# Optimization experiments

Hardware: AMD Instinct MI355X
Metric: run time of the kernel (lower is better)

## Reference

```python
import jax, jax.numpy as jnp
import numpy as np

N_NODES, D_NODE = 100000, 128
N_EDGES, D_EDGE = 1000000, 32
D_IN = 2 * D_NODE + D_EDGE  # 288
H1, H2, D_OUT = 128, 64, 1


def setup_inputs() -> dict:
    key = jax.random.key(0)
    ks = jax.random.split(key, 9)
    x = jax.random.normal(ks[0], (N_NODES, D_NODE), dtype=jnp.float32)
    edge_index = jax.random.randint(ks[1], (2, N_EDGES), 0, N_NODES, dtype=jnp.int64)
    edge_features = jax.random.normal(ks[2], (N_EDGES, D_EDGE), dtype=jnp.float32)
    def lin(kw, kb, fan_in, fan_out):
        bound = 1.0 / np.sqrt(fan_in)
        W = jax.random.uniform(kw, (fan_in, fan_out), minval=-bound, maxval=bound, dtype=jnp.float32)
        b = jax.random.uniform(kb, (fan_out,), minval=-bound, maxval=bound, dtype=jnp.float32)
        return W, b
    W1, b1 = lin(ks[3], ks[4], D_IN, H1)
    W2, b2 = lin(ks[5], ks[6], H1, H2)
    W3, b3 = lin(ks[7], ks[8], H2, D_OUT)
    return {"x": x, "edge_index": edge_index, "edge_features": edge_features,
            "W1": W1, "b1": b1, "W2": W2, "b2": b2, "W3": W3, "b3": b3}


def reference(x, edge_index, edge_features, W1, b1, W2, b2, W3, b3):
    origin, destination = edge_index[0], edge_index[1]
    # [E, 2*D_NODE + D_EDGE]
    z = jnp.concatenate([x[origin], x[destination], edge_features], axis=1)
    z = jax.nn.leaky_relu(z @ W1 + b1)  # negative_slope=0.01, matches torch default
    z = jax.nn.leaky_relu(z @ W2 + b2)
    z = z @ W3 + b3
    return z.reshape(-1)
```

## Files before the change

kernel.cpp:

```cpp
#include <hip/hip_runtime.h>

#define N_NODES 100000
#define N_EDGES 1000000

typedef __attribute__((ext_vector_type(8))) short bf16x8;
typedef __attribute__((ext_vector_type(4))) float f32x4;
typedef __attribute__((ext_vector_type(4))) unsigned u32x4;

static __device__ __forceinline__ short f2bf(float f) {
    unsigned u = __float_as_uint(f);
    u = (u + 0x7fffu + ((u >> 16) & 1u)) >> 16;
    return (short)u;
}
static __device__ __forceinline__ float bf2f(unsigned short s) {
    return __uint_as_float(((unsigned)s) << 16);
}
static __device__ __forceinline__ float lrelu(float x) {
    return fmaxf(x, 0.01f * x);
}
static __device__ __forceinline__ unsigned cvtpk(float lo, float hi) {
    unsigned r;
    asm("v_cvt_pk_bf16_f32 %0, %1, %2" : "=v"(r) : "v"(lo), "v"(hi));
    return r;
}

__global__ __launch_bounds__(256) void precompute_mfma(
    const float* __restrict__ x, const float* __restrict__ W1,
    const float* __restrict__ b1, unsigned short* __restrict__ Pb,
    unsigned short* __restrict__ Qb)
{
    const int t    = threadIdx.x;
    const int lane = t & 63;
    const int w    = t >> 6;
    const int q    = lane >> 4;
    const int n15  = lane & 15;
    const int chb  = 64 * w;

    bf16x8 afrag[4][4];
    #pragma unroll
    for (int mtl = 0; mtl < 4; ++mtl) {
        const int ch = chb + 16 * mtl + n15;
        const float* wcol = (ch < 128) ? (W1 + ch) : (W1 + 128 * 128 + (ch - 128));
        #pragma unroll
        for (int ks = 0; ks < 4; ++ks)
            #pragma unroll
            for (int j = 0; j < 8; ++j)
                afrag[mtl][ks][j] = f2bf(wcol[(size_t)(32 * ks + 8 * q + j) * 128]);
    }
    float b1r[16];
    #pragma unroll
    for (int mtl = 0; mtl < 4; ++mtl)
        #pragma unroll
        for (int r = 0; r < 4; ++r) {
            const int ch = chb + 16 * mtl + 4 * q + r;
            b1r[mtl * 4 + r] = (ch < 128) ? b1[ch] : 0.0f;
        }

    unsigned short* tbase = (w < 2) ? Pb : Qb;
    const int mtb = 4 * (w & 1);

    for (int tile = blockIdx.x; tile < N_NODES / 16; tile += gridDim.x) {
        const int n0 = tile * 16;
        const float* xrow = x + (size_t)(n0 + n15) * 128;

        bf16x8 bfr[4];
        #pragma unroll
        for (int ks = 0; ks < 4; ++ks) {
            f32x4 xa = *(const f32x4*)(xrow + 32 * ks + 8 * q);
            f32x4 xb = *(const f32x4*)(xrow + 32 * ks + 8 * q + 4);
            u32x4 bu;
            bu[0] = cvtpk(xa[0], xa[1]);
            bu[1] = cvtpk(xa[2], xa[3]);
            bu[2] = cvtpk(xb[0], xb[1]);
            bu[3] = cvtpk(xb[2], xb[3]);
            bfr[ks] = __builtin_bit_cast(bf16x8, bu);
        }
        #pragma unroll
        for (int mtl = 0; mtl < 4; ++mtl) {
            f32x4 acc = {0.f, 0.f, 0.f, 0.f};
            #pragma unroll
            for (int ks = 0; ks < 4; ++ks)
                acc = __builtin_amdgcn_mfma_f32_16x16x32_bf16(afrag[mtl][ks], bfr[ks], acc, 0, 0, 0);
            unsigned* dst = (unsigned*)(tbase + (size_t)(n0 + n15) * 128 + q * 32 + (mtb + mtl) * 4);
            dst[0] = cvtpk(acc[0] + b1r[mtl * 4 + 0], acc[1] + b1r[mtl * 4 + 1]);
            dst[1] = cvtpk(acc[2] + b1r[mtl * 4 + 2], acc[3] + b1r[mtl * 4 + 3]);
        }
    }
}

__global__ __launch_bounds__(256, 3) void edge_mfma(
    const int* __restrict__ ei, const float* __restrict__ ef,
    const float* __restrict__ W1, const float* __restrict__ W2,
    const float* __restrict__ b2, const float* __restrict__ W3,
    const float* __restrict__ b3, const unsigned short* __restrict__ Pb,
    const unsigned short* __restrict__ Qb, float* __restrict__ out)
{
    __shared__ unsigned short w2s[16 * 64 * 8];
    __shared__ unsigned short a1s[8 * 64 * 8];
    const int t    = threadIdx.x;
    const int lane = t & 63;
    const int w    = t >> 6;
    const int q    = lane >> 4;
    const int n15  = lane & 15;

    #pragma unroll
    for (int i = 0; i < 2; ++i) {
        const int mt = 2 * w + i;
        bf16x8 f;
        #pragma unroll
        for (int j = 0; j < 8; ++j)
            f[j] = f2bf(W1[(size_t)(256 + 8 * q + j) * 128 + 16 * mt + n15]);
        *(bf16x8*)&a1s[(mt * 64 + lane) * 8] = f;
    }

    {
        const int mt2 = w;
        #pragma unroll
        for (int ks = 0; ks < 4; ++ks) {
            bf16x8 f;
            #pragma unroll
            for (int j = 0; j < 8; ++j) {
                const int ch = 32 * ks + ((j < 4) ? (4 * q + j) : (16 + 4 * q + (j - 4)));
                f[j] = f2bf(W2[(size_t)ch * 64 + 16 * mt2 + n15]);
            }
            *(bf16x8*)&w2s[(((mt2 << 2) | ks) * 64 + lane) * 8] = f;
        }
    }

    unsigned b2w3[16];
    #pragma unroll
    for (int mt2 = 0; mt2 < 4; ++mt2)
        #pragma unroll
        for (int r = 0; r < 4; ++r) {
            const int ch = 16 * mt2 + 4 * q + r;
            b2w3[mt2 * 4 + r] = (unsigned)(unsigned short)f2bf(b2[ch])
                              | ((unsigned)(unsigned short)f2bf(W3[ch]) << 16);
        }
    const float b3v = b3[0];

    __syncthreads();

    const int nTiles  = N_EDGES / 16;
    const int wid     = blockIdx.x * 4 + w;
    const int wstride = gridDim.x * 4;
    if (wid >= nTiles) return;

    int t0 = wid, t1 = t0 + wstride, t2 = t1 + wstride;
    bool h1 = t1 < nTiles, h2 = t2 < nTiles;

    int oi0, di0, oi1, di1, oi2, di2;
    f32x4 ea0, eb0, ea1, eb1, ea2, eb2;
    {
        const int e0 = t0 * 16;
        oi0 = ei[e0 + n15];
        di0 = ei[N_EDGES + e0 + n15];
        ea0 = *(const f32x4*)(ef + (size_t)(e0 + n15) * 32 + 8 * q);
        eb0 = *(const f32x4*)(ef + (size_t)(e0 + n15) * 32 + 8 * q + 4);
    }
    oi1 = oi0; di1 = di0; ea1 = ea0; eb1 = eb0;
    if (h1) {
        const int e1 = t1 * 16;
        oi1 = ei[e1 + n15];
        di1 = ei[N_EDGES + e1 + n15];
        ea1 = *(const f32x4*)(ef + (size_t)(e1 + n15) * 32 + 8 * q);
        eb1 = *(const f32x4*)(ef + (size_t)(e1 + n15) * 32 + 8 * q + 4);
    }
    oi2 = oi1; di2 = di1; ea2 = ea1; eb2 = eb1;
    if (h2) {
        const int e2 = t2 * 16;
        oi2 = ei[e2 + n15];
        di2 = ei[N_EDGES + e2 + n15];
        ea2 = *(const f32x4*)(ef + (size_t)(e2 + n15) * 32 + 8 * q);
        eb2 = *(const f32x4*)(ef + (size_t)(e2 + n15) * 32 + 8 * q + 4);
    }

    bf16x8 pvbA[4], qvbA[4], pvbB[4], qvbB[4];
    {
        const unsigned short* prow = Pb + (size_t)oi0 * 128 + q * 32;
        const unsigned short* qrow = Qb + (size_t)di0 * 128 + q * 32;
        #pragma unroll
        for (int c = 0; c < 4; ++c) {
            pvbA[c] = *(const bf16x8*)(prow + 8 * c);
            qvbA[c] = *(const bf16x8*)(qrow + 8 * c);
        }
    }
    if (h1) {
        const unsigned short* prow = Pb + (size_t)oi1 * 128 + q * 32;
        const unsigned short* qrow = Qb + (size_t)di1 * 128 + q * 32;
        #pragma unroll
        for (int c = 0; c < 4; ++c) {
            pvbB[c] = *(const bf16x8*)(prow + 8 * c);
            qvbB[c] = *(const bf16x8*)(qrow + 8 * c);
        }
    } else {
        #pragma unroll
        for (int c = 0; c < 4; ++c) { pvbB[c] = pvbA[c]; qvbB[c] = qvbA[c]; }
    }

#define STEP(PC, QC)                                                           \
    {                                                                          \
        u32x4 befu;                                                            \
        befu[0] = cvtpk(ea0[0], ea0[1]);                                       \
        befu[1] = cvtpk(ea0[2], ea0[3]);                                       \
        befu[2] = cvtpk(eb0[0], eb0[1]);                                       \
        befu[3] = cvtpk(eb0[2], eb0[3]);                                       \
        const bf16x8 bef = __builtin_bit_cast(bf16x8, befu);                   \
        const int  t3 = t2 + wstride;                                          \
        const bool h3 = h2 && (t3 < nTiles);                                   \
        int oi3 = oi2, di3 = di2;                                              \
        f32x4 ea3 = ea2, eb3 = eb2;                                            \
        if (h3) {                                                              \
            const int e3 = t3 * 16;                                            \
            oi3 = ei[e3 + n15];                                                \
            di3 = ei[N_EDGES + e3 + n15];                                      \
            ea3 = *(const f32x4*)(ef + (size_t)(e3 + n15) * 32 + 8 * q);       \
            eb3 = *(const f32x4*)(ef + (size_t)(e3 + n15) * 32 + 8 * q + 4);   \
        }                                                                      \
        \
        u32x4 hfu[4];                                                          \
        _Pragma("unroll")                                                      \
        for (int mt = 0; mt < 8; ++mt) {                                       \
            const bf16x8 a1f = *(const bf16x8*)&a1s[(mt * 64 + lane) * 8];     \
            f32x4 z = {0.f, 0.f, 0.f, 0.f};                                    \
            f32x4 hh = __builtin_amdgcn_mfma_f32_16x16x32_bf16(a1f, bef, z, 0, 0, 0); \
            const int c = mt >> 1, off = (mt & 1) * 4;                         \
            float v0 = lrelu(hh[0] + bf2f((unsigned short)PC[c][off + 0]) + bf2f((unsigned short)QC[c][off + 0])); \
            float v1 = lrelu(hh[1] + bf2f((unsigned short)PC[c][off + 1]) + bf2f((unsigned short)QC[c][off + 1])); \
            float v2 = lrelu(hh[2] + bf2f((unsigned short)PC[c][off + 2]) + bf2f((unsigned short)QC[c][off + 2])); \
            float v3 = lrelu(hh[3] + bf2f((unsigned short)PC[c][off + 3]) + bf2f((unsigned short)QC[c][off + 3])); \
            hfu[mt >> 1][(mt & 1) * 2 + 0] = cvtpk(v0, v1);                    \
            hfu[mt >> 1][(mt & 1) * 2 + 1] = cvtpk(v2, v3);                    \
        }                                                                      \
        \
        \
        if (h2) {                                                              \
            const unsigned short* prow = Pb + (size_t)oi2 * 128 + q * 32;      \
            const unsigned short* qrow = Qb + (size_t)di2 * 128 + q * 32;      \
            _Pragma("unroll")                                                  \
            for (int c2 = 0; c2 < 4; ++c2) {                                   \
                PC[c2] = *(const bf16x8*)(prow + 8 * c2);                      \
                QC[c2] = *(const bf16x8*)(qrow + 8 * c2);                      \
            }                                                                  \
        }                                                                      \
                  \
        f32x4 acc2[4] = {{0.f,0.f,0.f,0.f},{0.f,0.f,0.f,0.f},{0.f,0.f,0.f,0.f},{0.f,0.f,0.f,0.f}}; \
        _Pragma("unroll")                                                      \
        for (int ks = 0; ks < 4; ++ks) {                                       \
            const bf16x8 hfrag = __builtin_bit_cast(bf16x8, hfu[ks]);          \
            _Pragma("unroll")                                                  \
            for (int mt2 = 0; mt2 < 4; ++mt2) {                                \
                const bf16x8 a2f = *(const bf16x8*)&w2s[(((mt2 << 2) | ks) * 64 + lane) * 8]; \
                acc2[mt2] = __builtin_amdgcn_mfma_f32_16x16x32_bf16(a2f, hfrag, acc2[mt2], 0, 0, 0); \
            }                                                                  \
        }                                                                      \
                          \
        float s = 0.0f;                                                        \
        _Pragma("unroll")                                                      \
        for (int mt2 = 0; mt2 < 4; ++mt2)                                      \
            _Pragma("unroll")                                                  \
            for (int r = 0; r < 4; ++r) {                                      \
                const unsigned u = b2w3[mt2 * 4 + r];                          \
                float v = acc2[mt2][r] + bf2f((unsigned short)(u & 0xffffu));  \
                v = lrelu(v);                                                  \
                s += v * __uint_as_float(u & 0xffff0000u);                     \
            }                                                                  \
        s += __shfl_xor(s, 16);                                                \
        s += __shfl_xor(s, 32);                                                \
        if (q == 0) out[t0 * 16 + n15] = s + b3v;                              \
        if (!h1) goto done;                                                    \
        t0 = t1; t1 = t2; t2 = t3;                                             \
        h1 = h2; h2 = h3;                                                      \
        ea0 = ea1; eb0 = eb1; ea1 = ea2; eb1 = eb2; ea2 = ea3; eb2 = eb3;      \
        oi2 = oi3; di2 = di3;                                                  \
    }

    for (;;) {
        STEP(pvbA, qvbA);
        STEP(pvbB, qvbB);
    }
done: ;
#undef STEP
}

extern "C" void kernel_launch(void* const* d_in, const int* in_sizes, int n_in,
                              void* d_out, int out_size, void* d_ws, size_t ws_size,
                              hipStream_t stream) {
    const float* x   = (const float*)d_in[0];
    const int*   ei  = (const int*)d_in[1];
    const float* ef  = (const float*)d_in[2];
    const float* W1  = (const float*)d_in[3];
    const float* b1  = (const float*)d_in[4];
    const float* W2  = (const float*)d_in[5];
    const float* b2  = (const float*)d_in[6];
    const float* W3  = (const float*)d_in[7];
    const float* b3  = (const float*)d_in[8];
    float*       out = (float*)d_out;

    unsigned short* Pb = (unsigned short*)d_ws;
    unsigned short* Qb = Pb + (size_t)N_NODES * 128;

    precompute_mfma<<<2048, 256, 0, stream>>>(x, W1, b1, Pb, Qb);
    edge_mfma<<<768, 256, 0, stream>>>(ei, ef, W1, W2, b2, W3, b3, Pb, Qb, out);
}
```

Measured before the change: 356.6 us.

## Shorten edge prefetch pipeline, issue gathers at step start, use nontemporal streaming loads

Cuts the edge-index and edge-feature software pipeline from three tiles ahead to two. The P/Q row gathers for the next tile now issue at the start of each step instead of after the layer-1 MFMAs, and the ping-pong buffers are swapped accordingly. Streaming reads of x, edge indices and edge features, plus the output store, become nontemporal so they are less likely to evict the gathered P/Q rows from cache. The precompute grid shrinks from 2048 to 512 blocks. The shorter pipeline lowers register pressure but gives each load less latency cover.

```diff
diff --git a/kernel.cpp b/kernel.cpp
--- a/kernel.cpp
+++ b/kernel.cpp
@@ -22,6 +22,12 @@
     unsigned r;
     asm("v_cvt_pk_bf16_f32 %0, %1, %2" : "=v"(r) : "v"(lo), "v"(hi));
     return r;
+}
+static __device__ __forceinline__ f32x4 ldnt_f4(const float* p) {
+    return __builtin_nontemporal_load((const f32x4*)p);
+}
+static __device__ __forceinline__ int ldnt_i(const int* p) {
+    return __builtin_nontemporal_load(p);
 }
 
 __global__ __launch_bounds__(256) void precompute_mfma(
@@ -66,8 +72,8 @@
         bf16x8 bfr[4];
         #pragma unroll
         for (int ks = 0; ks < 4; ++ks) {
-            f32x4 xa = *(const f32x4*)(xrow + 32 * ks + 8 * q);
-            f32x4 xb = *(const f32x4*)(xrow + 32 * ks + 8 * q + 4);
+            f32x4 xa = ldnt_f4(xrow + 32 * ks + 8 * q);
+            f32x4 xb = ldnt_f4(xrow + 32 * ks + 8 * q + 4);
             u32x4 bu;
             bu[0] = cvtpk(xa[0], xa[1]);
             bu[1] = cvtpk(xa[2], xa[3]);
@@ -145,33 +151,25 @@
     const int wstride = gridDim.x * 4;
     if (wid >= nTiles) return;
 
-    int t0 = wid, t1 = t0 + wstride, t2 = t1 + wstride;
-    bool h1 = t1 < nTiles, h2 = t2 < nTiles;
-
-    int oi0, di0, oi1, di1, oi2, di2;
-    f32x4 ea0, eb0, ea1, eb1, ea2, eb2;
+    int tile0 = wid;
+    int tile1 = tile0 + wstride;
+    bool have1 = tile1 < nTiles;
+
+    int oi0, di0; f32x4 ea0, eb0;
     {
-        const int e0 = t0 * 16;
-        oi0 = ei[e0 + n15];
-        di0 = ei[N_EDGES + e0 + n15];
-        ea0 = *(const f32x4*)(ef + (size_t)(e0 + n15) * 32 + 8 * q);
-        eb0 = *(const f32x4*)(ef + (size_t)(e0 + n15) * 32 + 8 * q + 4);
-    }
-    oi1 = oi0; di1 = di0; ea1 = ea0; eb1 = eb0;
-    if (h1) {
-        const int e1 = t1 * 16;
-        oi1 = ei[e1 + n15];
-        di1 = ei[N_EDGES + e1 + n15];
-        ea1 = *(const f32x4*)(ef + (size_t)(e1 + n15) * 32 + 8 * q);
-        eb1 = *(const f32x4*)(ef + (size_t)(e1 + n15) * 32 + 8 * q + 4);
-    }
-    oi2 = oi1; di2 = di1; ea2 = ea1; eb2 = eb1;
-    if (h2) {
-        const int e2 = t2 * 16;
-        oi2 = ei[e2 + n15];
-        di2 = ei[N_EDGES + e2 + n15];
-        ea2 = *(const f32x4*)(ef + (size_t)(e2 + n15) * 32 + 8 * q);
-        eb2 = *(const f32x4*)(ef + (size_t)(e2 + n15) * 32 + 8 * q + 4);
+        const int e0 = tile0 * 16;
+        oi0 = ldnt_i(&ei[e0 + n15]);
+        di0 = ldnt_i(&ei[N_EDGES + e0 + n15]);
+        ea0 = ldnt_f4(ef + (size_t)(e0 + n15) * 32 + 8 * q);
+        eb0 = ldnt_f4(ef + (size_t)(e0 + n15) * 32 + 8 * q + 4);
+    }
+    int oi1 = oi0, di1 = di0; f32x4 ea1 = ea0, eb1 = eb0;
+    if (have1) {
+        const int e1 = tile1 * 16;
+        oi1 = ldnt_i(&ei[e1 + n15]);
+        di1 = ldnt_i(&ei[N_EDGES + e1 + n15]);
+        ea1 = ldnt_f4(ef + (size_t)(e1 + n15) * 32 + 8 * q);
+        eb1 = ldnt_f4(ef + (size_t)(e1 + n15) * 32 + 8 * q + 4);
     }
 
     bf16x8 pvbA[4], qvbA[4], pvbB[4], qvbB[4];
@@ -184,39 +182,38 @@
             qvbA[c] = *(const bf16x8*)(qrow + 8 * c);
         }
     }
-    if (h1) {
-        const unsigned short* prow = Pb + (size_t)oi1 * 128 + q * 32;
-        const unsigned short* qrow = Qb + (size_t)di1 * 128 + q * 32;
-        #pragma unroll
-        for (int c = 0; c < 4; ++c) {
-            pvbB[c] = *(const bf16x8*)(prow + 8 * c);
-            qvbB[c] = *(const bf16x8*)(qrow + 8 * c);
-        }
-    } else {
-        #pragma unroll
-        for (int c = 0; c < 4; ++c) { pvbB[c] = pvbA[c]; qvbB[c] = qvbA[c]; }
-    }
-
-#define STEP(PC, QC)                                                           \
+    #pragma unroll
+    for (int c = 0; c < 4; ++c) { pvbB[c] = pvbA[c]; qvbB[c] = qvbA[c]; }
+
+#define STEP(PC, QC, PN, QN)                                                   \
     {                                                                          \
+        if (have1) {                                                           \
+            const unsigned short* prow = Pb + (size_t)oi1 * 128 + q * 32;      \
+            const unsigned short* qrow = Qb + (size_t)di1 * 128 + q * 32;      \
+            _Pragma("unroll")                                                  \
+            for (int c2 = 0; c2 < 4; ++c2) {                                   \
+                PN[c2] = *(const bf16x8*)(prow + 8 * c2);                      \
+                QN[c2] = *(const bf16x8*)(qrow + 8 * c2);                      \
+            }                                                                  \
+        }                                                                      \
         u32x4 befu;                                                            \
         befu[0] = cvtpk(ea0[0], ea0[1]);                                       \
         befu[1] = cvtpk(ea0[2], ea0[3]);                                       \
         befu[2] = cvtpk(eb0[0], eb0[1]);                                       \
         befu[3] = cvtpk(eb0[2], eb0[3]);                                       \
         const bf16x8 bef = __builtin_bit_cast(bf16x8, befu);                   \
-        const int  t3 = t2 + wstride;                                          \
-        const bool h3 = h2 && (t3 < nTiles);                                   \
-        int oi3 = oi2, di3 = di2;                                              \
-        f32x4 ea3 = ea2, eb3 = eb2;                                            \
-        if (h3) {                                                              \
-            const int e3 = t3 * 16;                                            \
-            oi3 = ei[e3 + n15];                                                \
-            di3 = ei[N_EDGES + e3 + n15];                                      \
-            ea3 = *(const f32x4*)(ef + (size_t)(e3 + n15) * 32 + 8 * q);       \
-            eb3 = *(const f32x4*)(ef + (size_t)(e3 + n15) * 32 + 8 * q + 4);   \
-        }                                                                      \
-        \
+        const int  tile2 = tile1 + wstride;                                    \
+        const bool have2 = have1 && (tile2 < nTiles);                          \
+        int oi2 = oi1, di2 = di1;                                              \
+        f32x4 ea2 = ea1, eb2 = eb1;                                            \
+        if (have2) {                                                           \
+            const int e2 = tile2 * 16;                                         \
+            oi2 = ldnt_i(&ei[e2 + n15]);                                       \
+            di2 = ldnt_i(&ei[N_EDGES + e2 + n15]);                             \
+            ea2 = ldnt_f4(ef + (size_t)(e2 + n15) * 32 + 8 * q);               \
+            eb2 = ldnt_f4(ef + (size_t)(e2 + n15) * 32 + 8 * q + 4);           \
+        }                                                                      \
+            \
         u32x4 hfu[4];                                                          \
         _Pragma("unroll")                                                      \
         for (int mt = 0; mt < 8; ++mt) {                                       \
@@ -231,17 +228,6 @@
             hfu[mt >> 1][(mt & 1) * 2 + 0] = cvtpk(v0, v1);                    \
             hfu[mt >> 1][(mt & 1) * 2 + 1] = cvtpk(v2, v3);                    \
         }                                                                      \
-        \
-        \
-        if (h2) {                                                              \
-            const unsigned short* prow = Pb + (size_t)oi2 * 128 + q * 32;      \
-            const unsigned short* qrow = Qb + (size_t)di2 * 128 + q * 32;      \
-            _Pragma("unroll")                                                  \
-            for (int c2 = 0; c2 < 4; ++c2) {                                   \
-                PC[c2] = *(const bf16x8*)(prow + 8 * c2);                      \
-                QC[c2] = *(const bf16x8*)(qrow + 8 * c2);                      \
-            }                                                                  \
-        }                                                                      \
                   \
         f32x4 acc2[4] = {{0.f,0.f,0.f,0.f},{0.f,0.f,0.f,0.f},{0.f,0.f,0.f,0.f},{0.f,0.f,0.f,0.f}}; \
         _Pragma("unroll")                                                      \
@@ -266,17 +252,16 @@
             }                                                                  \
         s += __shfl_xor(s, 16);                                                \
         s += __shfl_xor(s, 32);                                                \
-        if (q == 0) out[t0 * 16 + n15] = s + b3v;                              \
-        if (!h1) goto done;                                                    \
-        t0 = t1; t1 = t2; t2 = t3;                                             \
-        h1 = h2; h2 = h3;                                                      \
-        ea0 = ea1; eb0 = eb1; ea1 = ea2; eb1 = eb2; ea2 = ea3; eb2 = eb3;      \
-        oi2 = oi3; di2 = di3;                                                  \
+        if (q == 0) __builtin_nontemporal_store(s + b3v, &out[tile0 * 16 + n15]); \
+        if (!have1) goto done;                                                 \
+        tile0 = tile1; tile1 = tile2; have1 = have2;                           \
+        oi1 = oi2; di1 = di2;                                                  \
+        ea0 = ea1; eb0 = eb1; ea1 = ea2; eb1 = eb2;                            \
     }
 
     for (;;) {
-        STEP(pvbA, qvbA);
-        STEP(pvbB, qvbB);
+        STEP(pvbA, qvbA, pvbB, qvbB);
+        STEP(pvbB, qvbB, pvbA, qvbA);
     }
 done: ;
 #undef STEP
@@ -299,6 +284,6 @@
     unsigned short* Pb = (unsigned short*)d_ws;
     unsigned short* Qb = Pb + (size_t)N_NODES * 128;
 
-    precompute_mfma<<<2048, 256, 0, stream>>>(x, W1, b1, Pb, Qb);
+    precompute_mfma<<<512, 256, 0, stream>>>(x, W1, b1, Pb, Qb);
     edge_mfma<<<768, 256, 0, stream>>>(ei, ef, W1, W2, b2, W3, b3, Pb, Qb, out);
 }
```

New measurement: 341.4 us. -4.3%, faster.
